# Performance work log

Hardware: AMD Instinct MI355X
Metric: run time of the kernel (lower is better)

The kernel has to match this reference:

```python
import jax, jax.numpy as jnp
import numpy as np

EMBED_DIM = 2048
Q_HEADS = 32
KV_HEADS = 8
HEAD_DIM = EMBED_DIM // Q_HEADS  # 64
REPEATS = Q_HEADS // KV_HEADS    # 4


def setup_inputs() -> dict:
    key = jax.random.key(0)
    ks = jax.random.split(key, 5)
    B, T = 2, 2048
    x = jax.random.normal(ks[0], (B, T, EMBED_DIM), dtype=jnp.float32)
    s = 1.0 / np.sqrt(EMBED_DIM)
    # torch nn.Linear weights are [out_features, in_features]
    Wq = jax.random.uniform(ks[1], (Q_HEADS * HEAD_DIM, EMBED_DIM), minval=-s, maxval=s, dtype=jnp.float32)
    Wk = jax.random.uniform(ks[2], (KV_HEADS * HEAD_DIM, EMBED_DIM), minval=-s, maxval=s, dtype=jnp.float32)
    Wv = jax.random.uniform(ks[3], (KV_HEADS * HEAD_DIM, EMBED_DIM), minval=-s, maxval=s, dtype=jnp.float32)
    Wo = jax.random.uniform(ks[4], (EMBED_DIM, Q_HEADS * HEAD_DIM), minval=-s, maxval=s, dtype=jnp.float32)
    return {"x": x, "Wq": Wq, "Wk": Wk, "Wv": Wv, "Wo": Wo}


def reference(x, Wq, Wk, Wv, Wo):
    B, T, C = x.shape
    # projections (x @ W.T), then split heads
    q = (x @ Wq.T).reshape(B, T, Q_HEADS, HEAD_DIM)
    k = (x @ Wk.T).reshape(B, T, KV_HEADS, HEAD_DIM)
    v = (x @ Wv.T).reshape(B, T, KV_HEADS, HEAD_DIM)
    # group query heads by shared kv head: [B, kvH, rep, T, d]
    q = q.transpose(0, 2, 1, 3).reshape(B, KV_HEADS, REPEATS, T, HEAD_DIM)
    k = k.transpose(0, 2, 1, 3)  # [B, kvH, T, d]
    v = v.transpose(0, 2, 1, 3)
    scale = 1.0 / np.sqrt(HEAD_DIM)
    # scores: [B, kvH, rep, Tq, Tk] -- KV shared across rep (no materialized repeat)
    scores = jnp.einsum('bgrtd,bgsd->bgrts', q, k) * scale
    causal = jnp.tril(jnp.ones((T, T), dtype=bool))
    scores = jnp.where(causal, scores, jnp.finfo(scores.dtype).min)
    attn = jax.nn.softmax(scores, axis=-1)
    y = jnp.einsum('bgrts,bgsd->bgrtd', attn, v)
    # [B, kvH, rep, T, d] -> [B, T, qH*d]
    y = y.reshape(B, Q_HEADS, T, HEAD_DIM).transpose(0, 2, 1, 3).reshape(B, T, Q_HEADS * HEAD_DIM)
    return y @ Wo.T
```

## Files before the change

kernel.cpp:

```cpp
#include <hip/hip_runtime.h>

#define BATCH 2
#define SEQ   2048
#define CDIM  2048
#define QH    32
#define KVH   8
#define HD    64

typedef __bf16 bf16x8 __attribute__((ext_vector_type(8)));
typedef float  f32x4  __attribute__((ext_vector_type(4)));
typedef float  f32x16 __attribute__((ext_vector_type(16)));
typedef unsigned int u32;

#define GAS __attribute__((address_space(1)))
#define LAS __attribute__((address_space(3)))

__device__ __forceinline__ void gload_lds16(const void* g, void* l) {
  __builtin_amdgcn_global_load_lds((const GAS void*)g, (LAS void*)l, 16, 0, 0);
}

__device__ __forceinline__ unsigned short f2bf(float f) {
  union { float fv; unsigned u; } v; v.fv = f;
  unsigned r = v.u + 0x7FFF + ((v.u >> 16) & 1);
  return (unsigned short)(r >> 16);
}

__device__ __forceinline__ float fastexp2(float x) {
#if __has_builtin(__builtin_amdgcn_exp2f)
  return __builtin_amdgcn_exp2f(x);
#else
  return exp2f(x);
#endif
}

__device__ __forceinline__ u32 cvtpk_bf16(float lo, float hi) {
  u32 r;
  asm("v_cvt_pk_bf16_f32 %0, %1, %2" : "=v"(r) : "v"(lo), "v"(hi));
  return r;
}

__device__ __forceinline__ void permswap(u32& a, u32& b) {
  asm volatile("v_permlane32_swap_b32 %0, %1" : "+v"(a), "+v"(b));
}

__global__ __launch_bounds__(256) void cvt_all(
    const float* __restrict__ x,  const float* __restrict__ wq,
    const float* __restrict__ wk, const float* __restrict__ wv,
    const float* __restrict__ wo,
    unsigned short* __restrict__ xb,  unsigned short* __restrict__ wqb,
    unsigned short* __restrict__ wkb, unsigned short* __restrict__ wvb,
    unsigned short* __restrict__ wob)
{
  const int i = blockIdx.x * 256 + threadIdx.x;
  const float* s; unsigned short* d; int o;
  if      (i < 1048576) { s = x;  d = xb;  o = i; }
  else if (i < 1572864) { s = wq; d = wqb; o = i - 1048576; }
  else if (i < 1703936) { s = wk; d = wkb; o = i - 1572864; }
  else if (i < 1835008) { s = wv; d = wvb; o = i - 1703936; }
  else                  { s = wo; d = wob; o = i - 1835008; }
  const f32x4* sp = (const f32x4*)(s + (long)o * 8);
  f32x4 a = sp[0], b = sp[1];
  union { unsigned short u[8]; bf16x8 v; } ov;
  #pragma unroll
  for (int j = 0; j < 4; j++) { ov.u[j] = f2bf(a[j]); ov.u[4 + j] = f2bf(b[j]); }
  *(bf16x8*)(d + (long)o * 8) = ov.v;
}


__global__ __launch_bounds__(512, 2) void gemm_qkv(
    const unsigned short* __restrict__ A,
    const unsigned short* __restrict__ W,
    unsigned short* __restrict__ O0,
    unsigned short* __restrict__ O1,
    unsigned short* __restrict__ O2)
{
  __shared__ unsigned short lds[57344];
  constexpr int K  = CDIM;
  constexpr int NT = K / 64;
  const int tid  = threadIdx.x;
  const int lane = tid & 63;
  const int l15  = lane & 15;
  const int lg   = lane >> 4;
  const int wid  = tid >> 6;
  const int wm   = wid >> 1;
  const int wn   = wid & 1;
  const int m0 = blockIdx.y * 256;
  const int n0 = blockIdx.x * 192;

  const unsigned short* Ag = A + (long)m0 * K;
  const unsigned short* Bg = W + (long)n0 * K;

  const int srow  = tid >> 3;
  const int scol8 = 8 * ((tid & 7) ^ (srow & 7));
  const int rswz  = (l15 & 7) << 3;

  f32x4 acc[4][6] = {};
  bf16x8 a[4][2], b[3][2];

#define SA(T)                                                                 \
  do {                                                                        \
    unsigned short* _d = &lds[(((T) & 1) * 28672) + tid * 8];                 \
    _Pragma("unroll")                                                         \
    for (int _pp = 0; _pp < 4; _pp++)                                         \
      gload_lds16(Ag + (long)(_pp * 64 + srow) * K + (T) * 64 + scol8,        \
                  _d + _pp * 4096);                                           \
  } while (0)

#define SB(T)                                                                 \
  do {                                                                        \
    unsigned short* _d = &lds[(((T) & 1) * 28672) + 16384 + tid * 8];         \
    _Pragma("unroll")                                                         \
    for (int _pp = 0; _pp < 3; _pp++)                                         \
      gload_lds16(Bg + (long)(_pp * 64 + srow) * K + (T) * 64 + scol8,        \
                  _d + _pp * 4096);                                           \
  } while (0)

#define LDA()                                                                 \
  _Pragma("unroll") for (int _mi = 0; _mi < 4; _mi++)                         \
  _Pragma("unroll") for (int _kk = 0; _kk < 2; _kk++) {                       \
    const int _row = wm * 64 + _mi * 16 + l15;                                \
    const int _ce = (_kk * 32 + lg * 8) ^ rswz;                               \
    a[_mi][_kk] = *(const bf16x8*)&lds[bufb + _row * 64 + _ce];               \
  }

#define LDB(NH)                                                               \
  _Pragma("unroll") for (int _ni = 0; _ni < 3; _ni++)                         \
  _Pragma("unroll") for (int _kk = 0; _kk < 2; _kk++) {                       \
    const int _row = wn * 96 + ((NH) * 3 + _ni) * 16 + l15;                   \
    const int _ce = (_kk * 32 + lg * 8) ^ rswz;                               \
    b[_ni][_kk] = *(const bf16x8*)&lds[bufb + 16384 + _row * 64 + _ce];       \
  }

#define MFMAQ(NH)                                                             \
  do {                                                                        \
    __builtin_amdgcn_s_setprio(1);                                            \
    _Pragma("unroll") for (int _mi = 0; _mi < 4; _mi++)                       \
    _Pragma("unroll") for (int _ni = 0; _ni < 3; _ni++)                       \
    _Pragma("unroll") for (int _kk = 0; _kk < 2; _kk++)                       \
      acc[_mi][(NH) * 3 + _ni] =                                              \
        __builtin_amdgcn_mfma_f32_16x16x32_bf16(                              \
          a[_mi][_kk], b[_ni][_kk], acc[_mi][(NH) * 3 + _ni], 0, 0, 0);       \
    __builtin_amdgcn_s_setprio(0);                                            \
  } while (0)

#define BAR()                                                                 \
  do { __builtin_amdgcn_sched_barrier(0); __builtin_amdgcn_s_barrier(); } while (0)

  SA(0); SB(0); SA(1);
  asm volatile("s_waitcnt vmcnt(4)" ::: "memory");
  BAR();

  for (int t = 0; t < NT; t++) {
    const int bufb = (t & 1) * 28672;
    if (t + 1 < NT) SB(t + 1);
    LDA(); LDB(0);
    BAR();
    if (t + 2 < NT) SA(t + 2);
    MFMAQ(0);
    LDB(1);
    MFMAQ(1);
    if (t + 2 < NT) asm volatile("s_waitcnt vmcnt(4)" ::: "memory");
    else            asm volatile("s_waitcnt vmcnt(0)" ::: "memory");
    BAR();
  }
#undef SA
#undef SB
#undef LDA
#undef LDB
#undef MFMAQ

  const int bb = m0 >> 11, t0 = m0 & 2047;
  const int vstart = (n0 > 2560) ? n0 : 2560;
  const int nV = n0 + 192 - vstart;
  char* ldsb = (char*)lds;
  #pragma unroll
  for (int mi = 0; mi < 4; mi++) {
    const int rg0 = wm * 64 + mi * 16 + lg * 4;
    #pragma unroll
    for (int ni = 0; ni < 6; ni++) {
      const int cg = n0 + wn * 96 + ni * 16 + l15;
      if (cg < 2048) {
        const int hh = cg >> 6, dd = cg & 63;
        #pragma unroll
        for (int r = 0; r < 4; r++)
          O0[(((long)(bb * QH + hh)) * SEQ + t0 + rg0 + r) * HD + dd] =
              f2bf(acc[mi][ni][r]);
      } else if (cg < 2560) {
        const int nn = cg - 2048, gg = nn >> 6, dd = nn & 63;
        #pragma unroll
        for (int r = 0; r < 4; r++)
          O1[(((long)(bb * KVH + gg)) * SEQ + t0 + rg0 + r) * HD + dd] =
              f2bf(acc[mi][ni][r]);
      } else {
        const int cglV = cg - vstart;
        uint2 pk;
        pk.x = cvtpk_bf16(acc[mi][ni][0], acc[mi][ni][1]);
        pk.y = cvtpk_bf16(acc[mi][ni][2], acc[mi][ni][3]);
        const int byte = cglV * 512 + ((rg0 * 2) ^ ((cglV & 31) << 4));
        *(uint2*)(ldsb + byte) = pk;
      }
    }
  }
  if (nV > 0) {
    __syncthreads();
    const int nn0 = vstart - 2560;
    for (int it = 0; it < nV / 16; it++) {
      const int cglV = it * 16 + (tid >> 5);
      const int tch = tid & 31;
      const int byte = cglV * 512 + ((tch * 16) ^ ((cglV & 31) << 4));
      uint4 vv = *(uint4*)(ldsb + byte);
      const int nn = nn0 + cglV, gg = nn >> 6, dd = nn & 63;
      *(uint4*)(O2 + (((long)(bb * KVH + gg)) * HD + dd) * SEQ + t0 + tch * 8) = vv;
    }
  }
#undef BAR
}

__global__ __launch_bounds__(512, 2) void gemm_wo(
    const unsigned short* __restrict__ A,
    const unsigned short* __restrict__ W0,
    float* __restrict__ Of)
{
  __shared__ unsigned short lds[49152];
  constexpr int K  = CDIM;
  constexpr int NT = K / 64;
  const int tid  = threadIdx.x;
  const int lane = tid & 63;
  const int l15  = lane & 15;
  const int lg   = lane >> 4;
  const int wid  = tid >> 6;
  const int wm   = wid >> 2;
  const int wn   = wid & 3;
  const int m0 = blockIdx.y * 256;
  const int n0 = blockIdx.x * 128;

  const unsigned short* Ag = A  + (long)m0 * K;
  const unsigned short* Bg = W0 + (long)n0 * K;

  const int srow  = tid >> 3;
  const int scol8 = 8 * ((tid & 7) ^ (srow & 7));
  const int rswz  = (l15 & 7) << 3;

  f32x4 acc[8][2] = {};
  bf16x8 a[4][2], b[2][2];

#define STAGEA(H, T)                                                          \
  do {                                                                        \
    const int _rb = (H) * 128 + srow;                                         \
    unsigned short* _d = &lds[((T) & 1) * 24576 + (H) * 8192 + tid * 8];      \
    gload_lds16(Ag + (long)_rb * K + (T) * 64 + scol8, _d);                   \
    gload_lds16(Ag + (long)(_rb + 64) * K + (T) * 64 + scol8, _d + 4096);     \
  } while (0)

#define STAGEB(T)                                                             \
  do {                                                                        \
    unsigned short* _d = &lds[((T) & 1) * 24576 + 16384 + tid * 8];           \
    gload_lds16(Bg + (long)srow * K + (T) * 64 + scol8, _d);                  \
    gload_lds16(Bg + (long)(srow + 64) * K + (T) * 64 + scol8, _d + 4096);    \
  } while (0)

#define LDA(MH)                                                               \
  _Pragma("unroll") for (int _mi = 0; _mi < 4; _mi++)                         \
  _Pragma("unroll") for (int _kk = 0; _kk < 2; _kk++) {                       \
    const int _row = wm * 64 + _mi * 16 + l15;                                \
    const int _ce = (_kk * 32 + lg * 8) ^ rswz;                               \
    a[_mi][_kk] = *(const bf16x8*)&lds[bufb + (MH) * 8192 + _row * 64 + _ce]; \
  }

#define LDBW()                                                                \
  _Pragma("unroll") for (int _ni = 0; _ni < 2; _ni++)                         \
  _Pragma("unroll") for (int _kk = 0; _kk < 2; _kk++) {                       \
    const int _row = wn * 32 + _ni * 16 + l15;                                \
    const int _ce = (_kk * 32 + lg * 8) ^ rswz;                               \
    b[_ni][_kk] = *(const bf16x8*)&lds[bufb + 16384 + _row * 64 + _ce];       \
  }

#define MFMAH(MH)                                                             \
  do {                                                                        \
    __builtin_amdgcn_s_setprio(1);                                            \
    _Pragma("unroll") for (int _mi = 0; _mi < 4; _mi++)                       \
    _Pragma("unroll") for (int _ni = 0; _ni < 2; _ni++)                       \
    _Pragma("unroll") for (int _kk = 0; _kk < 2; _kk++)                       \
      acc[(MH) * 4 + _mi][_ni] =                                              \
        __builtin_amdgcn_mfma_f32_16x16x32_bf16(                              \
          a[_mi][_kk], b[_ni][_kk], acc[(MH) * 4 + _mi][_ni], 0, 0, 0);       \
    __builtin_amdgcn_s_setprio(0);                                            \
  } while (0)

#define BAR()                                                                 \
  do { __builtin_amdgcn_sched_barrier(0); __builtin_amdgcn_s_barrier(); } while (0)

  STAGEA(0, 0); STAGEB(0); STAGEA(1, 0);
  STAGEA(0, 1); STAGEA(1, 1);
  asm volatile("s_waitcnt vmcnt(4)" ::: "memory");
  BAR();

  for (int t = 0; t < NT; t++) {
    const int bufb = (t & 1) * 24576;
    LDA(0); LDBW();
    if (t + 1 < NT) STAGEB(t + 1);
    BAR();
    if (t + 2 < NT) STAGEA(0, t + 2);
    MFMAH(0);
    LDA(1);
    BAR();
    if (t + 2 < NT) STAGEA(1, t + 2);
    MFMAH(1);
    if (t + 2 < NT) asm volatile("s_waitcnt vmcnt(4)" ::: "memory");
    else            asm volatile("s_waitcnt vmcnt(0)" ::: "memory");
    BAR();
  }
#undef STAGEA
#undef STAGEB
#undef LDA
#undef LDBW
#undef MFMAH
#undef BAR

  #pragma unroll
  for (int mi = 0; mi < 8; mi++) {
    const int rbase = m0 + (mi >> 2) * 128 + wm * 64 + (mi & 3) * 16 + lg * 4;
    #pragma unroll
    for (int ni = 0; ni < 2; ni++) {
      const int cg = n0 + wn * 32 + ni * 16 + l15;
      #pragma unroll
      for (int r = 0; r < 4; r++)
        Of[(long)(rbase + r) * 2048 + cg] = acc[mi][ni][r];
    }
  }
}

__global__ __launch_bounds__(256, 3) void attn_kernel(
    const unsigned short* __restrict__ q,
    const unsigned short* __restrict__ k,
    const unsigned short* __restrict__ vt,
    unsigned short* __restrict__ y)
{
  __shared__ unsigned short Ks[2][4096];
  __shared__ unsigned short Vs[2][4096];
  __shared__ unsigned short Ytile[4][32][72];
  const int tid  = threadIdx.x;
  const int lane = tid & 63;
  const int l31  = lane & 31;
  const int lg2  = lane >> 5;
  const int w    = tid >> 6;

  const int idx = blockIdx.x;
  const int r   = idx & 7;
  const int s   = idx >> 3;
  const int j   = 15 - (s >> 3);
  const int qs  = s & 7;
  const int c   = r + ((qs & 1) << 3);
  const int g   = c >> 1;
  const int b   = c & 1;
  const int h   = g * 4 + (qs >> 1);

  const unsigned short* kbase = k  + ((long)(b * KVH + g)) * SEQ * HD;
  const unsigned short* vbase = vt + ((long)(b * KVH + g)) * HD * SEQ;
  const float kscale = 0.125f * 1.44269504088896340736f;
  const int fswz = (l31 & 7) << 3;

#define STAGE(T, CUR)                                                          \
  do {                                                                         \
    const int _tk = (T) << 6;                                                  \
    _Pragma("unroll")                                                          \
    for (int _c = 0; _c < 2; _c++) {                                           \
      const int _idx = (w * 2 + _c) * 64 + lane;                               \
      const int _row = _idx >> 3;                                              \
      const int _sw  = ((_idx & 7) * 8) ^ ((_row & 7) << 3);                   \
      gload_lds16(kbase + (long)(_tk + _row) * HD + _sw, &Ks[CUR][_idx * 8]);  \
      gload_lds16(vbase + (long)_row * SEQ + _tk + _sw, &Vs[CUR][_idx * 8]);   \
    }                                                                          \
  } while (0)

#define STEP(T, CUR)                                                           \
  do {                                                                         \
    bf16x8 kf[8];                                                              \
    _Pragma("unroll")                                                          \
    for (int _j = 0; _j < 2; _j++)                                             \
      _Pragma("unroll")                                                        \
      for (int _dc = 0; _dc < 4; _dc++)                                        \
        kf[_j * 4 + _dc] = *(const bf16x8*)&Ks[CUR][(_j * 32 + l31) * 64 +     \
                               ((_dc * 16 + lg2 * 8) ^ fswz)];                 \
    f32x16 st0 = {}, st1 = {};                                                 \
    __builtin_amdgcn_s_setprio(1);                                             \
    _Pragma("unroll")                                                          \
    for (int _dc = 0; _dc < 4; _dc++) {                                        \
      st0 = __builtin_amdgcn_mfma_f32_32x32x16_bf16(kf[_dc],     qf[_dc], st0, 0, 0, 0); \
      st1 = __builtin_amdgcn_mfma_f32_32x32x16_bf16(kf[4 + _dc], qf[_dc], st1, 0, 0, 0); \
    }                                                                          \
    __builtin_amdgcn_s_setprio(0);                                             \
    float s2[32];                                                              \
    if ((T) == n64w - 1) {                                                     \
      const int _thr = mthr + l31;                                             \
      _Pragma("unroll")                                                        \
      for (int _r = 0; _r < 16; _r++) {                                        \
        const int _kl = (_r & 3) + 8 * (_r >> 2) + 4 * lg2;                    \
        s2[_r]      = (_kl      > _thr) ? -__builtin_inff() : st0[_r];         \
        s2[16 + _r] = (_kl + 32 > _thr) ? -__builtin_inff() : st1[_r];         \
      }                                                                        \
    } else {                                                                   \
      _Pragma("unroll")                                                        \
      for (int _r = 0; _r < 16; _r++) {                                        \
        s2[_r] = st0[_r]; s2[16 + _r] = st1[_r];                               \
      }                                                                        \
    }                                                                          \
    float _m16[16], _m8[8], _m4[4];                                            \
    _Pragma("unroll")                                                          \
    for (int _i = 0; _i < 16; _i++) _m16[_i] = fmaxf(s2[_i], s2[_i + 16]);     \
    _Pragma("unroll")                                                          \
    for (int _i = 0; _i < 8; _i++) _m8[_i] = fmaxf(_m16[_i], _m16[_i + 8]);    \
    _Pragma("unroll")                                                          \
    for (int _i = 0; _i < 4; _i++) _m4[_i] = fmaxf(_m8[_i], _m8[_i + 4]);      \
    float _pm = fmaxf(fmaxf(_m4[0], _m4[1]), fmaxf(_m4[2], _m4[3]));           \
    _pm = fmaxf(_pm, __shfl_xor(_pm, 32));                                     \
    if (!__all(_pm <= mrow + 44.3614195558f)) {                                \
      const float _fs = fastexp2((mrow - _pm) * kscale);                       \
      mrow = _pm; lrow *= _fs;                                                 \
      _Pragma("unroll")                                                        \
      for (int _r = 0; _r < 16; _r++) { yacc0[_r] *= _fs; yacc1[_r] *= _fs; }  \
    }                                                                          \
    const float _nc = mrow * kscale;                                           \
    _Pragma("unroll")                                                          \
    for (int _r = 0; _r < 32; _r++)                                            \
      s2[_r] = fastexp2(__builtin_fmaf(s2[_r], kscale, -_nc));                 \
    float _a16[16], _a8[8], _a4[4];                                            \
    _Pragma("unroll")                                                          \
    for (int _i = 0; _i < 16; _i++) _a16[_i] = s2[_i] + s2[_i + 16];           \
    _Pragma("unroll")                                                          \
    for (int _i = 0; _i < 8; _i++) _a8[_i] = _a16[_i] + _a16[_i + 8];          \
    _Pragma("unroll")                                                          \
    for (int _i = 0; _i < 4; _i++) _a4[_i] = _a8[_i] + _a8[_i + 4];            \
    float _sum = (_a4[0] + _a4[1]) + (_a4[2] + _a4[3]);                        \
    _sum += __shfl_xor(_sum, 32);                                              \
    lrow += _sum;                                                              \
    union { u32 u[4]; bf16x8 v; } _pb[4];                                      \
    _Pragma("unroll")                                                          \
    for (int _jj = 0; _jj < 2; _jj++) {                                        \
      const int _o = _jj * 16;                                                 \
      u32 _w0 = cvtpk_bf16(s2[_o + 0],  s2[_o + 1]);                           \
      u32 _w1 = cvtpk_bf16(s2[_o + 2],  s2[_o + 3]);                           \
      u32 _w2 = cvtpk_bf16(s2[_o + 4],  s2[_o + 5]);                           \
      u32 _w3 = cvtpk_bf16(s2[_o + 6],  s2[_o + 7]);                           \
      u32 _w4 = cvtpk_bf16(s2[_o + 8],  s2[_o + 9]);                           \
      u32 _w5 = cvtpk_bf16(s2[_o + 10], s2[_o + 11]);                          \
      u32 _w6 = cvtpk_bf16(s2[_o + 12], s2[_o + 13]);                          \
      u32 _w7 = cvtpk_bf16(s2[_o + 14], s2[_o + 15]);                          \
      permswap(_w0, _w2); permswap(_w1, _w3);                                  \
      permswap(_w4, _w6); permswap(_w5, _w7);                                  \
      _pb[_jj * 2].u[0] = _w0; _pb[_jj * 2].u[1] = _w1;                        \
      _pb[_jj * 2].u[2] = _w2; _pb[_jj * 2].u[3] = _w3;                        \
      _pb[_jj * 2 + 1].u[0] = _w4; _pb[_jj * 2 + 1].u[1] = _w5;                \
      _pb[_jj * 2 + 1].u[2] = _w6; _pb[_jj * 2 + 1].u[3] = _w7;                \
    }                                                                          \
    bf16x8 vf[8];                                                              \
    _Pragma("unroll")                                                          \
    for (int _c = 0; _c < 4; _c++) {                                           \
      vf[_c * 2]     = *(const bf16x8*)&Vs[CUR][l31 * 64 +                     \
                           ((_c * 16 + lg2 * 8) ^ fswz)];                      \
      vf[_c * 2 + 1] = *(const bf16x8*)&Vs[CUR][(32 + l31) * 64 +              \
                           ((_c * 16 + lg2 * 8) ^ fswz)];                      \
    }                                                                          \
    __builtin_amdgcn_s_setprio(1);                                             \
    _Pragma("unroll")                                                          \
    for (int _c = 0; _c < 4; _c++) {                                           \
      yacc0 = __builtin_amdgcn_mfma_f32_32x32x16_bf16(vf[_c * 2],     _pb[_c].v, yacc0, 0, 0, 0); \
      yacc1 = __builtin_amdgcn_mfma_f32_32x32x16_bf16(vf[_c * 2 + 1], _pb[_c].v, yacc1, 0, 0, 0); \
    }                                                                          \
    __builtin_amdgcn_s_setprio(0);                                             \
  } while (0)

  const int i      = 4 * j + w;
  const int q0     = i * 32;
  const int n64w   = (i >> 1) + 1;
  const int n64max = 2 * j + 2;
  const int mthr   = (i & 1) ? 32 : 0;
  const unsigned short* qbase = q + (((long)(b * QH + h)) * SEQ + q0) * HD;

  bf16x8 qf[4];
  #pragma unroll
  for (int dc = 0; dc < 4; dc++)
    qf[dc] = *(const bf16x8*)(qbase + (long)l31 * HD + dc * 16 + (lg2 << 3));

  float mrow = -__builtin_inff(), lrow = 0.f;
  f32x16 yacc0 = {}, yacc1 = {};

  STAGE(0, 0);
  int cur = 0;
  for (int t = 0; t < n64max; t++) {
    __syncthreads();
    if (t + 1 < n64max) STAGE(t + 1, cur ^ 1);
    if (t < n64w) STEP(t, cur);
    cur ^= 1;
  }

  const float rl = 1.f / lrow;
  #pragma unroll
  for (int r2 = 0; r2 < 16; r2++) {
    const int dv = (r2 & 3) + 8 * (r2 >> 2) + 4 * lg2;
    Ytile[w][l31][dv]      = f2bf(yacc0[r2] * rl);
    Ytile[w][l31][32 + dv] = f2bf(yacc1[r2] * rl);
  }
  asm volatile("s_waitcnt lgkmcnt(0)" ::: "memory");
  __builtin_amdgcn_sched_barrier(0);
  #pragma unroll
  for (int it = 0; it < 4; it++) {
    const int qr = it * 8 + (lane >> 3);
    const int dc = (lane & 7) * 8;
    bf16x8 vv = *(const bf16x8*)&Ytile[w][qr][dc];
    *(bf16x8*)(y + (((long)b * SEQ + q0 + qr) * QH + h) * HD + dc) = vv;
  }
#undef STAGE
#undef STEP
}

extern "C" void kernel_launch(void* const* d_in, const int* in_sizes, int n_in,
                              void* d_out, int out_size, void* d_ws, size_t ws_size,
                              hipStream_t stream) {
  const float* xf  = (const float*)d_in[0];
  const float* Wqf = (const float*)d_in[1];
  const float* Wkf = (const float*)d_in[2];
  const float* Wvf = (const float*)d_in[3];
  const float* Wof = (const float*)d_in[4];

  const int nx  = 8388608;
  const int nwq = 4194304;
  const int nwk = 1048576;
  const int nwv = 1048576;
  const int nwo = 4194304;

  unsigned short* ws  = (unsigned short*)d_ws;
  unsigned short* xb  = ws;
  unsigned short* Wqb = xb  + nx;
  unsigned short* Wkb = Wqb + nwq;
  unsigned short* Wvb = Wkb + nwk;
  unsigned short* Wob = Wvb + nwv;
  unsigned short* qb  = Wob + nwo;
  unsigned short* kb  = qb  + 8388608;
  unsigned short* vtb = kb  + 2097152;
  unsigned short* yb  = vtb + 2097152;
  float* ob = (float*)d_out;

  cvt_all<<<dim3(9216), dim3(256), 0, stream>>>(xf, Wqf, Wkf, Wvf, Wof,
                                                xb, Wqb, Wkb, Wvb, Wob);
  gemm_qkv<<<dim3(16, 16), dim3(512), 0, stream>>>(xb, Wqb, qb, kb, vtb);
  attn_kernel<<<dim3(1024), dim3(256), 0, stream>>>(qb, kb, vtb, yb);
  gemm_wo<<<dim3(16, 16), dim3(512), 0, stream>>>(yb, Wob, ob);
}
```

Measured before the change: 155.0 us.

## Pair mirrored causal query tiles per block to balance work and share K/V

Each attention block now handles two query tiles, one near the start and its mirror near the end of the sequence, so every block carries the same causal work. The K and V tiles staged in LDS and the fragments loaded into registers are shared by both tiles. Grid size is halved and launch bounds drop to 2 blocks per CU, since register use grows with two sets of accumulators and softmax state. This removes the causal load imbalance and halves K/V staging traffic, at the cost of fewer resident waves and more register pressure.

```diff
diff --git a/kernel.cpp b/kernel.cpp
--- a/kernel.cpp
+++ b/kernel.cpp
@@ -330,7 +330,7 @@
   }
 }
 
-__global__ __launch_bounds__(256, 3) void attn_kernel(
+__global__ __launch_bounds__(256, 2) void attn_kernel(
     const unsigned short* __restrict__ q,
     const unsigned short* __restrict__ k,
     const unsigned short* __restrict__ vt,
@@ -348,7 +348,7 @@
   const int idx = blockIdx.x;
   const int r   = idx & 7;
   const int s   = idx >> 3;
-  const int j   = 15 - (s >> 3);
+  const int j   = s >> 3;
   const int qs  = s & 7;
   const int c   = r + ((qs & 1) << 3);
   const int g   = c >> 1;
@@ -359,6 +359,8 @@
   const unsigned short* vbase = vt + ((long)(b * KVH + g)) * HD * SEQ;
   const float kscale = 0.125f * 1.44269504088896340736f;
   const int fswz = (l31 & 7) << 3;
+
+  union PBU { u32 u[4]; bf16x8 v; };
 
 #define STAGE(T, CUR)                                                          \
   do {                                                                         \
@@ -373,36 +375,49 @@
     }                                                                          \
   } while (0)
 
-#define STEP(T, CUR)                                                           \
+#define LOADKF(CUR)                                                            \
+  _Pragma("unroll")                                                            \
+  for (int _jj = 0; _jj < 2; _jj++)                                            \
+    _Pragma("unroll")                                                          \
+    for (int _dc = 0; _dc < 4; _dc++)                                          \
+      kf[_jj * 4 + _dc] = *(const bf16x8*)&Ks[CUR][(_jj * 32 + l31) * 64 +     \
+                              ((_dc * 16 + lg2 * 8) ^ fswz)];
+
+#define LOADVF(CUR)                                                            \
+  _Pragma("unroll")                                                            \
+  for (int _c = 0; _c < 4; _c++) {                                             \
+    vf[_c * 2]     = *(const bf16x8*)&Vs[CUR][l31 * 64 +                       \
+                         ((_c * 16 + lg2 * 8) ^ fswz)];                        \
+    vf[_c * 2 + 1] = *(const bf16x8*)&Vs[CUR][(32 + l31) * 64 +                \
+                         ((_c * 16 + lg2 * 8) ^ fswz)];                        \
+  }
+
+#define QKT(ST0, ST1, QF)                                                      \
   do {                                                                         \
-    bf16x8 kf[8];                                                              \
-    _Pragma("unroll")                                                          \
-    for (int _j = 0; _j < 2; _j++)                                             \
-      _Pragma("unroll")                                                        \
-      for (int _dc = 0; _dc < 4; _dc++)                                        \
-        kf[_j * 4 + _dc] = *(const bf16x8*)&Ks[CUR][(_j * 32 + l31) * 64 +     \
-                               ((_dc * 16 + lg2 * 8) ^ fswz)];                 \
-    f32x16 st0 = {}, st1 = {};                                                 \
     __builtin_amdgcn_s_setprio(1);                                             \
     _Pragma("unroll")                                                          \
     for (int _dc = 0; _dc < 4; _dc++) {                                        \
-      st0 = __builtin_amdgcn_mfma_f32_32x32x16_bf16(kf[_dc],     qf[_dc], st0, 0, 0, 0); \
-      st1 = __builtin_amdgcn_mfma_f32_32x32x16_bf16(kf[4 + _dc], qf[_dc], st1, 0, 0, 0); \
+      ST0 = __builtin_amdgcn_mfma_f32_32x32x16_bf16(kf[_dc],     QF[_dc], ST0, 0, 0, 0); \
+      ST1 = __builtin_amdgcn_mfma_f32_32x32x16_bf16(kf[4 + _dc], QF[_dc], ST1, 0, 0, 0); \
     }                                                                          \
     __builtin_amdgcn_s_setprio(0);                                             \
+  } while (0)
+
+#define SOFT(T, ST0, ST1, PB, MROW, LROW, YA0, YA1, NW, MTHR)                  \
+  do {                                                                         \
     float s2[32];                                                              \
-    if ((T) == n64w - 1) {                                                     \
-      const int _thr = mthr + l31;                                             \
+    if ((T) == (NW) - 1) {                                                     \
+      const int _thr = (MTHR) + l31;                                           \
       _Pragma("unroll")                                                        \
       for (int _r = 0; _r < 16; _r++) {                                        \
         const int _kl = (_r & 3) + 8 * (_r >> 2) + 4 * lg2;                    \
-        s2[_r]      = (_kl      > _thr) ? -__builtin_inff() : st0[_r];         \
-        s2[16 + _r] = (_kl + 32 > _thr) ? -__builtin_inff() : st1[_r];         \
+        s2[_r]      = (_kl      > _thr) ? -__builtin_inff() : ST0[_r];         \
+        s2[16 + _r] = (_kl + 32 > _thr) ? -__builtin_inff() : ST1[_r];         \
       }                                                                        \
     } else {                                                                   \
       _Pragma("unroll")                                                        \
       for (int _r = 0; _r < 16; _r++) {                                        \
-        s2[_r] = st0[_r]; s2[16 + _r] = st1[_r];                               \
+        s2[_r] = ST0[_r]; s2[16 + _r] = ST1[_r];                               \
       }                                                                        \
     }                                                                          \
     float _m16[16], _m8[8], _m4[4];                                            \
@@ -414,13 +429,13 @@
     for (int _i = 0; _i < 4; _i++) _m4[_i] = fmaxf(_m8[_i], _m8[_i + 4]);      \
     float _pm = fmaxf(fmaxf(_m4[0], _m4[1]), fmaxf(_m4[2], _m4[3]));           \
     _pm = fmaxf(_pm, __shfl_xor(_pm, 32));                                     \
-    if (!__all(_pm <= mrow + 44.3614195558f)) {                                \
-      const float _fs = fastexp2((mrow - _pm) * kscale);                       \
-      mrow = _pm; lrow *= _fs;                                                 \
+    if (!__all(_pm <= (MROW) + 44.3614195558f)) {                              \
+      const float _fs = fastexp2(((MROW) - _pm) * kscale);                     \
+      MROW = _pm; LROW *= _fs;                                                 \
       _Pragma("unroll")                                                        \
-      for (int _r = 0; _r < 16; _r++) { yacc0[_r] *= _fs; yacc1[_r] *= _fs; }  \
-    }                                                                          \
-    const float _nc = mrow * kscale;                                           \
+      for (int _r = 0; _r < 16; _r++) { YA0[_r] *= _fs; YA1[_r] *= _fs; }      \
+    }                                                                          \
+    const float _nc = (MROW) * kscale;                                         \
     _Pragma("unroll")                                                          \
     for (int _r = 0; _r < 32; _r++)                                            \
       s2[_r] = fastexp2(__builtin_fmaf(s2[_r], kscale, -_nc));                 \
@@ -433,8 +448,7 @@
     for (int _i = 0; _i < 4; _i++) _a4[_i] = _a8[_i] + _a8[_i + 4];            \
     float _sum = (_a4[0] + _a4[1]) + (_a4[2] + _a4[3]);                        \
     _sum += __shfl_xor(_sum, 32);                                              \
-    lrow += _sum;                                                              \
-    union { u32 u[4]; bf16x8 v; } _pb[4];                                      \
+    LROW += _sum;                                                              \
     _Pragma("unroll")                                                          \
     for (int _jj = 0; _jj < 2; _jj++) {                                        \
       const int _o = _jj * 16;                                                 \
@@ -448,70 +462,99 @@
       u32 _w7 = cvtpk_bf16(s2[_o + 14], s2[_o + 15]);                          \
       permswap(_w0, _w2); permswap(_w1, _w3);                                  \
       permswap(_w4, _w6); permswap(_w5, _w7);                                  \
-      _pb[_jj * 2].u[0] = _w0; _pb[_jj * 2].u[1] = _w1;                        \
-      _pb[_jj * 2].u[2] = _w2; _pb[_jj * 2].u[3] = _w3;                        \
-      _pb[_jj * 2 + 1].u[0] = _w4; _pb[_jj * 2 + 1].u[1] = _w5;                \
-      _pb[_jj * 2 + 1].u[2] = _w6; _pb[_jj * 2 + 1].u[3] = _w7;                \
-    }                                                                          \
-    bf16x8 vf[8];                                                              \
+      PB[_jj * 2].u[0] = _w0; PB[_jj * 2].u[1] = _w1;                          \
+      PB[_jj * 2].u[2] = _w2; PB[_jj * 2].u[3] = _w3;                          \
+      PB[_jj * 2 + 1].u[0] = _w4; PB[_jj * 2 + 1].u[1] = _w5;                  \
+      PB[_jj * 2 + 1].u[2] = _w6; PB[_jj * 2 + 1].u[3] = _w7;                  \
+    }                                                                          \
+  } while (0)
+
+#define PVX(PB, YA0, YA1)                                                      \
+  do {                                                                         \
+    __builtin_amdgcn_s_setprio(1);                                             \
     _Pragma("unroll")                                                          \
     for (int _c = 0; _c < 4; _c++) {                                           \
-      vf[_c * 2]     = *(const bf16x8*)&Vs[CUR][l31 * 64 +                     \
-                           ((_c * 16 + lg2 * 8) ^ fswz)];                      \
-      vf[_c * 2 + 1] = *(const bf16x8*)&Vs[CUR][(32 + l31) * 64 +              \
-                           ((_c * 16 + lg2 * 8) ^ fswz)];                      \
-    }                                                                          \
-    __builtin_amdgcn_s_setprio(1);                                             \
-    _Pragma("unroll")                                                          \
-    for (int _c = 0; _c < 4; _c++) {                                           \
-      yacc0 = __builtin_amdgcn_mfma_f32_32x32x16_bf16(vf[_c * 2],     _pb[_c].v, yacc0, 0, 0, 0); \
-      yacc1 = __builtin_amdgcn_mfma_f32_32x32x16_bf16(vf[_c * 2 + 1], _pb[_c].v, yacc1, 0, 0, 0); \
+      YA0 = __builtin_amdgcn_mfma_f32_32x32x16_bf16(vf[_c * 2],     PB[_c].v, YA0, 0, 0, 0); \
+      YA1 = __builtin_amdgcn_mfma_f32_32x32x16_bf16(vf[_c * 2 + 1], PB[_c].v, YA1, 0, 0, 0); \
     }                                                                          \
     __builtin_amdgcn_s_setprio(0);                                             \
   } while (0)
 
-  const int i      = 4 * j + w;
-  const int q0     = i * 32;
-  const int n64w   = (i >> 1) + 1;
-  const int n64max = 2 * j + 2;
-  const int mthr   = (i & 1) ? 32 : 0;
-  const unsigned short* qbase = q + (((long)(b * QH + h)) * SEQ + q0) * HD;
-
-  bf16x8 qf[4];
+#define EPI(Q0, LROW, YA0, YA1)                                                \
+  do {                                                                         \
+    const float _rl = 1.f / (LROW);                                            \
+    _Pragma("unroll")                                                          \
+    for (int _r2 = 0; _r2 < 16; _r2++) {                                       \
+      const int _dv = (_r2 & 3) + 8 * (_r2 >> 2) + 4 * lg2;                    \
+      Ytile[w][l31][_dv]      = f2bf(YA0[_r2] * _rl);                          \
+      Ytile[w][l31][32 + _dv] = f2bf(YA1[_r2] * _rl);                          \
+    }                                                                          \
+    asm volatile("s_waitcnt lgkmcnt(0)" ::: "memory");                         \
+    __builtin_amdgcn_sched_barrier(0);                                         \
+    _Pragma("unroll")                                                          \
+    for (int _it = 0; _it < 4; _it++) {                                        \
+      const int _qr = _it * 8 + (lane >> 3);                                   \
+      const int _dc2 = (lane & 7) * 8;                                         \
+      bf16x8 _vv = *(const bf16x8*)&Ytile[w][_qr][_dc2];                       \
+      *(bf16x8*)(y + (((long)b * SEQ + (Q0) + _qr) * QH + h) * HD + _dc2) = _vv; \
+    }                                                                          \
+  } while (0)
+
+  const int iA = 4 * j + w;
+  const int iB = 60 - 4 * j + w;
+  const int q0A = iA * 32, q0B = iB * 32;
+  const int nA = (iA >> 1) + 1;
+  const int nB = (iB >> 1) + 1;
+  const int n64max = 32 - 2 * j;
+  const int mthrA = (iA & 1) ? 32 : 0;
+  const int mthrB = (iB & 1) ? 32 : 0;
+
+  const unsigned short* qbaseA = q + (((long)(b * QH + h)) * SEQ + q0A) * HD;
+  const unsigned short* qbaseB = q + (((long)(b * QH + h)) * SEQ + q0B) * HD;
+
+  bf16x8 qfA[4], qfB[4];
   #pragma unroll
-  for (int dc = 0; dc < 4; dc++)
-    qf[dc] = *(const bf16x8*)(qbase + (long)l31 * HD + dc * 16 + (lg2 << 3));
-
-  float mrow = -__builtin_inff(), lrow = 0.f;
-  f32x16 yacc0 = {}, yacc1 = {};
+  for (int dc = 0; dc < 4; dc++) {
+    qfA[dc] = *(const bf16x8*)(qbaseA + (long)l31 * HD + dc * 16 + (lg2 << 3));
+    qfB[dc] = *(const bf16x8*)(qbaseB + (long)l31 * HD + dc * 16 + (lg2 << 3));
+  }
+
+  float mrowA = -__builtin_inff(), lrowA = 0.f;
+  float mrowB = -__builtin_inff(), lrowB = 0.f;
+  f32x16 yaccA0 = {}, yaccA1 = {};
+  f32x16 yaccB0 = {}, yaccB1 = {};
 
   STAGE(0, 0);
   int cur = 0;
   for (int t = 0; t < n64max; t++) {
     __syncthreads();
     if (t + 1 < n64max) STAGE(t + 1, cur ^ 1);
-    if (t < n64w) STEP(t, cur);
+    if (t < nB) {
+      bf16x8 kf[8], vf[8];
+      f32x16 stA0 = {}, stA1 = {}, stB0 = {}, stB1 = {};
+      PBU pbA[4], pbB[4];
+      const bool doA = t < nA;
+      LOADKF(cur);
+      if (doA) QKT(stA0, stA1, qfA);
+      QKT(stB0, stB1, qfB);
+      if (doA) SOFT(t, stA0, stA1, pbA, mrowA, lrowA, yaccA0, yaccA1, nA, mthrA);
+      LOADVF(cur);
+      SOFT(t, stB0, stB1, pbB, mrowB, lrowB, yaccB0, yaccB1, nB, mthrB);
+      if (doA) PVX(pbA, yaccA0, yaccA1);
+      PVX(pbB, yaccB0, yaccB1);
+    }
     cur ^= 1;
   }
 
-  const float rl = 1.f / lrow;
-  #pragma unroll
-  for (int r2 = 0; r2 < 16; r2++) {
-    const int dv = (r2 & 3) + 8 * (r2 >> 2) + 4 * lg2;
-    Ytile[w][l31][dv]      = f2bf(yacc0[r2] * rl);
-    Ytile[w][l31][32 + dv] = f2bf(yacc1[r2] * rl);
-  }
-  asm volatile("s_waitcnt lgkmcnt(0)" ::: "memory");
-  __builtin_amdgcn_sched_barrier(0);
-  #pragma unroll
-  for (int it = 0; it < 4; it++) {
-    const int qr = it * 8 + (lane >> 3);
-    const int dc = (lane & 7) * 8;
-    bf16x8 vv = *(const bf16x8*)&Ytile[w][qr][dc];
-    *(bf16x8*)(y + (((long)b * SEQ + q0 + qr) * QH + h) * HD + dc) = vv;
-  }
+  EPI(q0A, lrowA, yaccA0, yaccA1);
+  EPI(q0B, lrowB, yaccB0, yaccB1);
 #undef STAGE
-#undef STEP
+#undef LOADKF
+#undef LOADVF
+#undef QKT
+#undef SOFT
+#undef PVX
+#undef EPI
 }
 
 extern "C" void kernel_launch(void* const* d_in, const int* in_sizes, int n_in,
@@ -544,6 +587,6 @@
   cvt_all<<<dim3(9216), dim3(256), 0, stream>>>(xf, Wqf, Wkf, Wvf, Wof,
                                                 xb, Wqb, Wkb, Wvb, Wob);
   gemm_qkv<<<dim3(16, 16), dim3(512), 0, stream>>>(xb, Wqb, qb, kb, vtb);
-  attn_kernel<<<dim3(1024), dim3(256), 0, stream>>>(qb, kb, vtb, yb);
+  attn_kernel<<<dim3(512), dim3(256), 0, stream>>>(qb, kb, vtb, yb);
   gemm_wo<<<dim3(16, 16), dim3(512), 0, stream>>>(yb, Wob, ob);
 }
```

Result: no change. 158.0 us (+1.9%).
